# Optimization experiments

Measured on AMD Instinct MI355X. Metric: run time of the kernel, lower is better.

## Reference

```python
import jax, jax.numpy as jnp
import numpy as np

N_OER, N_CONCEPT, N_CLASS = 100000, 20000, 1000
F_ENT, HID = 64, 128
E_SR, E_EP, E_COV, E_BEL = 200000, 400000, 400000, 100000
NEG_SLOPE = 0.2


def _edges(k, n_src, n_dst, e):
    k1, k2 = jax.random.split(k)
    return jnp.stack([jax.random.randint(k1, (e,), 0, n_src),
                      jax.random.randint(k2, (e,), 0, n_dst)]).astype(jnp.int32)


def setup_inputs() -> dict:
    key = jax.random.key(0)
    ks = jax.random.split(key, 24)
    s = 0.05  # small init scale for numerically stable attention logits
    inp = {
        'x_oer': jax.random.normal(ks[0], (N_OER, F_ENT), jnp.float32),
        'x_concept': jax.random.normal(ks[1], (N_CONCEPT, F_ENT), jnp.float32),
        'x_class': jax.random.normal(ks[2], (N_CLASS, F_ENT), jnp.float32),
        'e_oer': jax.random.uniform(ks[3], (N_OER, F_ENT), jnp.float32),
        'e_concept': jax.random.uniform(ks[4], (N_CONCEPT, F_ENT), jnp.float32),
        'e_class': jax.random.uniform(ks[5], (N_CLASS, F_ENT), jnp.float32),
        'W_lin': jax.random.normal(ks[6], (3, F_ENT, HID), jnp.float32) * s,
        'b_lin': jnp.zeros((3, HID), jnp.float32),
        'Wsrc': jax.random.normal(ks[7], (2, 5, HID, HID), jnp.float32) * s,
        'Wdst': jax.random.normal(ks[8], (2, 5, HID, HID), jnp.float32) * s,
        'att_src': jax.random.normal(ks[9], (2, 5, HID), jnp.float32) * s,
        'att_dst': jax.random.normal(ks[10], (2, 5, HID), jnp.float32) * s,
        'b_gat': jnp.zeros((2, 5, HID), jnp.float32),
        'W_cls': jax.random.normal(ks[11], (2 * (F_ENT + HID), 1), jnp.float32) * s,
        'b_cls': jnp.zeros((1,), jnp.float32),
        'ei_before_sr': _edges(ks[12], N_OER, N_OER, E_SR),
        'ei_covers': _edges(ks[14], N_OER, N_CONCEPT, E_COV),
        'ei_belongs': _edges(ks[15], N_CONCEPT, N_CLASS, E_BEL),
        'ei_rev_covers': _edges(ks[16], N_CONCEPT, N_OER, E_COV),
        'ei_rev_belongs': _edges(ks[17], N_CLASS, N_CONCEPT, E_BEL),
    }
    # before_ep edges guaranteed self-loop-free (PyG removes then re-adds self loops)
    k1, k2 = jax.random.split(ks[13])
    src = jax.random.randint(k1, (E_EP,), 0, N_OER)
    dst = (src + jax.random.randint(k2, (E_EP,), 1, N_OER)) % N_OER
    inp['ei_before_ep'] = jnp.stack([src, dst]).astype(jnp.int32)
    return inp


def _gat(x_src, x_dst, src, dst, Ws, Wd, a_s, a_d, b, n_dst):
    # PyG GATConv, heads=1: h = xW (no bias); alpha = softmax_dst(leaky_relu(a_s.h_s[i] + a_d.h_d[j]))
    h_s = x_src @ Ws                                   # [Ns, C]
    h_d = x_dst @ Wd                                   # [Nd, C]
    logit = jax.nn.leaky_relu((h_s @ a_s)[src] + (h_d @ a_d)[dst], NEG_SLOPE)  # [E]
    m = jax.ops.segment_max(logit, dst, num_segments=n_dst)
    ex = jnp.exp(logit - m[dst])
    denom = jax.ops.segment_sum(ex, dst, num_segments=n_dst)
    alpha = ex / denom[dst]
    out = jax.ops.segment_sum(h_s[src] * alpha[:, None], dst, num_segments=n_dst)
    return out + b


def _forward(x_oer, x_concept, x_class, e_oer, e_concept, e_class,
             W_lin, b_lin, Wsrc, Wdst, att_src, att_dst, b_gat, W_cls, b_cls,
             ei_before_sr, ei_before_ep, ei_covers, ei_belongs,
             ei_rev_covers, ei_rev_belongs):
    # per-node-type input projection of the random embeddings
    h_oer = e_oer @ W_lin[0] + b_lin[0]
    h_con = e_concept @ W_lin[1] + b_lin[1]
    h_cls = e_class @ W_lin[2] + b_lin[2]

    # add self loops for OER->OER 'before_ep' (add_self_loops=True)
    loop = jnp.arange(N_OER, dtype=jnp.int32)
    ep_src = jnp.concatenate([ei_before_ep[0], loop])
    ep_dst = jnp.concatenate([ei_before_ep[1], loop])

    for l in range(2):
        P = lambda r: (Wsrc[l, r], Wdst[l, r], att_src[l, r], att_dst[l, r], b_gat[l, r])
        o_ep = _gat(h_oer, h_oer, ep_src, ep_dst, *P(0), N_OER)
        o_cov = _gat(h_oer, h_con, ei_covers[0], ei_covers[1], *P(1), N_CONCEPT)
        o_bel = _gat(h_con, h_cls, ei_belongs[0], ei_belongs[1], *P(2), N_CLASS)
        o_rcov = _gat(h_con, h_oer, ei_rev_covers[0], ei_rev_covers[1], *P(3), N_OER)
        o_rbel = _gat(h_cls, h_con, ei_rev_belongs[0], ei_rev_belongs[1], *P(4), N_CONCEPT)
        # HeteroConv aggr='mean' over edge types per destination node type
        h_oer = (o_ep + o_rcov) * 0.5
        h_con = (o_cov + o_rbel) * 0.5
        h_cls = o_bel

    n_oer = jnp.concatenate([x_oer, h_oer], axis=1)          # [N_OER, F_ENT+HID]
    feat = jnp.concatenate([n_oer[ei_before_sr[0]], n_oer[ei_before_sr[1]]], axis=1)
    return (feat @ W_cls + b_cls)[:, 0]                      # [E_SR]


def reference(x_oer, x_concept, x_class, e_oer, e_concept, e_class,
              W_lin, b_lin, Wsrc, Wdst, att_src, att_dst, b_gat, W_cls, b_cls,
              ei_before_sr, ei_before_ep, ei_covers, ei_belongs,
              ei_rev_covers, ei_rev_belongs):
    return _forward(x_oer, x_concept, x_class, e_oer, e_concept, e_class,
                    W_lin, b_lin, Wsrc, Wdst, att_src, att_dst, b_gat, W_cls, b_cls,
                    ei_before_sr, ei_before_ep, ei_covers, ei_belongs,
                    ei_rev_covers, ei_rev_belongs)
```

## Files before the change

kernel.cpp:

```cpp
#include <hip/hip_runtime.h>
#include <hip/hip_bf16.h>

#define NOER 100000
#define NCON 20000
#define NCLS 1000
#define FENT 64
#define HID 128
#define ESR 200000
#define EEP 400000
#define ECOV 400000
#define EBEL 100000
#define NEG 0.2f
#define NB_TOT 121000

#define SL0 0
#define SL1 NOER
#define SL2 (2*NOER)
#define SL3 (2*NOER + NCON)
#define SL4 (2*NOER + 2*NCON)
#define SL_TOT (2*NOER + 2*NCON + NCLS)
#define DL0 0
#define DL1 NOER
#define DL2 (NOER + NCON)
#define DL3 (NOER + NCON + NCLS)
#define DL4 (2*NOER + NCON + NCLS)
#define DL_TOT (2*NOER + 2*NCON + NCLS)
#define EX_TOT 1500000
#define SCAN_B1 ((DL_TOT + 255) / 256)

#define BSH 9
#define BWID (1 << BSH)
#define NBUCK ((DL_TOT + BWID - 1) / BWID)
#define EPB 4096
#define ABLK ((EX_TOT + EPB - 1) / EPB)

typedef unsigned short u16;
typedef unsigned int u32;
typedef short v8s __attribute__((ext_vector_type(8)));
typedef float v4f __attribute__((ext_vector_type(4)));

__device__ __forceinline__ float b2f(u32 bits) { return __uint_as_float(bits << 16); }
__device__ __forceinline__ u16 f2b(float x) {
    __hip_bfloat16 h = __float2bfloat16(x);
    return *(u16*)&h;
}
__device__ __forceinline__ float wredsum(float p) {
#pragma unroll
    for (int off = 32; off; off >>= 1) p += __shfl_down(p, off);
    return p;
}

__device__ __forceinline__ void edge_decode(int e, const int* __restrict__ ep,
                                            const int* __restrict__ cov,
                                            const int* __restrict__ bel,
                                            const int* __restrict__ rcov,
                                            const int* __restrict__ rbel,
                                            int& s, int& g) {
    if (e < 500000) {
        if (e < EEP) { s = ep[e]; g = DL0 + ep[EEP + e]; }
        else { s = e - EEP; g = DL0 + s; }
    } else if (e < 900000)  { int i = e - 500000;  s = cov[i];  g = DL1 + cov[ECOV + i]; }
    else if (e < 1000000)   { int i = e - 900000;  s = bel[i];  g = DL2 + bel[EBEL + i]; }
    else if (e < 1400000)   { int i = e - 1000000; s = rcov[i]; g = DL3 + rcov[ECOV + i]; }
    else                    { int i = e - 1400000; s = rbel[i]; g = DL4 + rbel[EBEL + i]; }
}

__global__ __launch_bounds__(256) void k_cntA(const int* __restrict__ ep, const int* __restrict__ cov,
                                              const int* __restrict__ bel, const int* __restrict__ rcov,
                                              const int* __restrict__ rbel, int* __restrict__ counts,
                                              int* __restrict__ bhm) {
    __shared__ int lh[NBUCK];
    for (int i = threadIdx.x; i < NBUCK; i += 256) lh[i] = 0;
    __syncthreads();
    int e0 = blockIdx.x * EPB;
    for (int k = 0; k < EPB; k += 256) {
        int e = e0 + k + threadIdx.x;
        if (e < EX_TOT) {
            int s, g;
            edge_decode(e, ep, cov, bel, rcov, rbel, s, g);
            atomicAdd(counts + g, 1);
            atomicAdd(&lh[g >> BSH], 1);
        }
    }
    __syncthreads();
    for (int i = threadIdx.x; i < NBUCK; i += 256) bhm[i * ABLK + blockIdx.x] = lh[i];
}

__global__ void k_scan1(const int* __restrict__ counts, int* __restrict__ part,
                        int* __restrict__ bsum) {
    __shared__ int sm[256];
    int i = blockIdx.x * 256 + threadIdx.x;
    int v = (i < DL_TOT) ? counts[i] : 0;
    sm[threadIdx.x] = v;
    __syncthreads();
#pragma unroll
    for (int off = 1; off < 256; off <<= 1) {
        int x = (threadIdx.x >= off) ? sm[threadIdx.x - off] : 0;
        __syncthreads();
        sm[threadIdx.x] += x;
        __syncthreads();
    }
    if (i < DL_TOT) part[i] = sm[threadIdx.x];
    if (threadIdx.x == 255) bsum[blockIdx.x] = sm[255];
}

__global__ void k_scan2(int* __restrict__ bsum) {
    __shared__ int sm[1024];
    int t = threadIdx.x;
    sm[t] = (t < SCAN_B1) ? bsum[t] : 0;
    __syncthreads();
#pragma unroll
    for (int off = 1; off < 1024; off <<= 1) {
        int x = (t >= off) ? sm[t - off] : 0;
        __syncthreads();
        sm[t] += x;
        __syncthreads();
    }
    if (t < SCAN_B1) bsum[t] = sm[t];
}

__global__ void k_scan3(const int* __restrict__ part, const int* __restrict__ bsum,
                        const int* __restrict__ counts, int* __restrict__ S,
                        int* __restrict__ cursor) {
    int i = blockIdx.x * 256 + threadIdx.x;
    if (i >= DL_TOT) return;
    int b = blockIdx.x;
    int s = part[i] + (b > 0 ? bsum[b - 1] : 0);
    S[i] = s;
    cursor[i] = s - counts[i];
}

__global__ void k_bscanA(const int* __restrict__ bhm, const int* __restrict__ cursor,
                         int* __restrict__ starts) {
    __shared__ int sm[256];
    __shared__ int carry;
    int u = blockIdx.x, t = threadIdx.x;
    if (t == 0) carry = 0;
    __syncthreads();
    int base = cursor[u << BSH];
    for (int c0 = 0; c0 < ABLK; c0 += 256) {
        int i = c0 + t;
        int v = (i < ABLK) ? bhm[u * ABLK + i] : 0;
        sm[t] = v;
        __syncthreads();
#pragma unroll
        for (int off = 1; off < 256; off <<= 1) {
            int x = (t >= off) ? sm[t - off] : 0;
            __syncthreads();
            sm[t] += x;
            __syncthreads();
        }
        if (i < ABLK) starts[u * ABLK + i] = base + carry + sm[t] - v;
        __syncthreads();
        if (t == 255) carry += sm[255];
        __syncthreads();
    }
}

__global__ __launch_bounds__(256) void k_bfillA(const int* __restrict__ ep, const int* __restrict__ cov,
                                                const int* __restrict__ bel, const int* __restrict__ rcov,
                                                const int* __restrict__ rbel,
                                                const int* __restrict__ starts, uint2* __restrict__ pairs) {
    __shared__ int lh[NBUCK];
    for (int i = threadIdx.x; i < NBUCK; i += 256) lh[i] = starts[i * ABLK + blockIdx.x];
    __syncthreads();
    int e0 = blockIdx.x * EPB;
    for (int k = 0; k < EPB; k += 256) {
        int e = e0 + k + threadIdx.x;
        if (e < EX_TOT) {
            int s, g;
            edge_decode(e, ep, cov, bel, rcov, rbel, s, g);
            int pos = atomicAdd(&lh[g >> BSH], 1);
            pairs[pos] = make_uint2((u32)s, (u32)g);
        }
    }
}

__global__ void k_fill2(const uint2* __restrict__ pairs, int* __restrict__ cursor,
                        int* __restrict__ csr) {
    int i = blockIdx.x * blockDim.x + threadIdx.x;
    if (i >= EX_TOT) return;
    uint2 p = pairs[i];
    int pos = atomicAdd(cursor + p.y, 1);
    csr[pos] = (int)p.x;
}

__device__ __forceinline__ int deg_bin(int d) { int b = d > 63 ? 63 : d; return 63 - b; }

__global__ void k_hist2(const int* __restrict__ counts, int* __restrict__ bh) {
    __shared__ int lh[64];
    if (threadIdx.x < 64) lh[threadIdx.x] = 0;
    __syncthreads();
    int g = blockIdx.x * 256 + threadIdx.x;
    if (g < DL_TOT) atomicAdd(&lh[deg_bin(counts[g])], 1);
    __syncthreads();
    if (threadIdx.x < 64) bh[threadIdx.x * SCAN_B1 + blockIdx.x] = lh[threadIdx.x];
}

__global__ void k_bscan(const int* __restrict__ bh, int* __restrict__ boff,
                        int* __restrict__ bintot) {
    __shared__ int sm[256];
    __shared__ int carry;
    int bin = blockIdx.x;
    if (threadIdx.x == 0) carry = 0;
    __syncthreads();
    for (int c0 = 0; c0 < SCAN_B1; c0 += 256) {
        int i = c0 + threadIdx.x;
        int v = (i < SCAN_B1) ? bh[bin * SCAN_B1 + i] : 0;
        sm[threadIdx.x] = v;
        __syncthreads();
#pragma unroll
        for (int off = 1; off < 256; off <<= 1) {
            int x = (threadIdx.x >= off) ? sm[threadIdx.x - off] : 0;
            __syncthreads();
            sm[threadIdx.x] += x;
            __syncthreads();
        }
        if (i < SCAN_B1) boff[bin * SCAN_B1 + i] = carry + sm[threadIdx.x] - v;
        __syncthreads();
        if (threadIdx.x == 255) carry += sm[255];
        __syncthreads();
    }
    if (threadIdx.x == 0) bintot[bin] = carry;
}

__global__ void k_hscan(const int* __restrict__ hist, int* __restrict__ bcur) {
    int t = threadIdx.x;
    int h = hist[t];
    int v = h;
#pragma unroll
    for (int off = 1; off < 64; off <<= 1) {
        int x = __shfl_up(v, off);
        if (t >= off) v += x;
    }
    bcur[t] = v - h;
}

__global__ void k_perm2(const int* __restrict__ counts, const int* __restrict__ binbase,
                        const int* __restrict__ boff, const int* __restrict__ S,
                        int* __restrict__ perm, int* __restrict__ segbeg,
                        int* __restrict__ segend) {
    __shared__ int lh[64];
    if (threadIdx.x < 64)
        lh[threadIdx.x] = binbase[threadIdx.x] + boff[threadIdx.x * SCAN_B1 + blockIdx.x];
    __syncthreads();
    int g = blockIdx.x * 256 + threadIdx.x;
    if (g >= DL_TOT) return;
    int c = counts[g];
    int se = S[g];
    int pos = atomicAdd(&lh[deg_bin(c)], 1);
    perm[pos] = g;
    segbeg[pos] = se - c;
    segend[pos] = se;
}

__global__ void k_cast(const float* __restrict__ e_oer, const float* __restrict__ e_con,
                       const float* __restrict__ e_cls, u16* __restrict__ eb) {
    int idx = blockIdx.x * blockDim.x + threadIdx.x;
    int i4 = idx * 4;
    if (i4 >= NB_TOT * FENT) return;
    const float* src;
    if (i4 < 6400000) src = e_oer + i4;
    else if (i4 < 7680000) src = e_con + (i4 - 6400000);
    else src = e_cls + (i4 - 7680000);
    float4 v = *(const float4*)src;
    u16* d = eb + i4;
    d[0] = f2b(v.x); d[1] = f2b(v.y); d[2] = f2b(v.z); d[3] = f2b(v.w);
}

__global__ void k_prep(const float* __restrict__ W_lin, const float* __restrict__ Wsrc,
                       const float* __restrict__ b_gat,
                       u16* __restrict__ Wlt, u16* __restrict__ Woer, u16* __restrict__ Wcon,
                       u16* __restrict__ Wcls, float* __restrict__ boer,
                       float* __restrict__ bcon, float* __restrict__ bcls2) {
    int i = blockIdx.x * 256 + threadIdx.x;
    if (i < 24576) {
        int t = i / 8192, r = i % 8192, c = r >> 6, k = r & 63;
        Wlt[i] = f2b(W_lin[t * 8192 + k * 128 + c]);
        return;
    }
    i -= 24576;
    if (i < 65536) {
        int l = i >> 15, r = i & 32767, c = r >> 8, k2 = r & 255;
        int rel = 5 * l + (k2 < 128 ? 0 : 3), k = k2 & 127;
        Woer[i] = f2b(Wsrc[(size_t)rel * 16384 + k * 128 + c]);
        return;
    }
    i -= 65536;
    if (i < 65536) {
        int l = i >> 15, r = i & 32767, c = r >> 8, k2 = r & 255;
        int rel = 5 * l + (k2 < 128 ? 1 : 4), k = k2 & 127;
        Wcon[i] = f2b(Wsrc[(size_t)rel * 16384 + k * 128 + c]);
        return;
    }
    i -= 65536;
    if (i < 32768) {
        int l = i >> 14, r = i & 16383, c = r >> 7, k = r & 127;
        Wcls[i] = f2b(Wsrc[(size_t)(5 * l + 2) * 16384 + k * 128 + c]);
        return;
    }
    i -= 32768;
    if (i < 256) { int l = i >> 7, c = i & 127;
        boer[i] = 0.5f * (b_gat[(5 * l + 0) * 128 + c] + b_gat[(5 * l + 3) * 128 + c]); return; }
    i -= 256;
    if (i < 256) { int l = i >> 7, c = i & 127;
        bcon[i] = 0.5f * (b_gat[(5 * l + 1) * 128 + c] + b_gat[(5 * l + 4) * 128 + c]); return; }
    i -= 256;
    if (i < 256) { int l = i >> 7, c = i & 127;
        bcls2[i] = b_gat[(5 * l + 2) * 128 + c]; }
}

__global__ void k_wvec(const float* __restrict__ Wsrc, const float* __restrict__ as_,
                       const float* __restrict__ Wdst, const float* __restrict__ ad,
                       float* __restrict__ wsv, float* __restrict__ wdv) {
    int a = blockIdx.x >> 5;
    int r = ((blockIdx.x & 31) << 2) + (threadIdx.x >> 6);
    int lane = threadIdx.x & 63;
    const float *W, *v;
    float* o;
    if (a < 10) { W = Wsrc + (size_t)a * HID * HID; v = as_ + a * HID; o = wsv + a * HID; }
    else { W = Wdst + (size_t)(a - 10) * HID * HID; v = ad + (a - 10) * HID; o = wdv + (a - 10) * HID; }
    float p = W[r * HID + lane] * v[lane] + W[r * HID + 64 + lane] * v[64 + lane];
    p = wredsum(p);
    if (lane == 0) o[r] = p;
}

struct GemmJob {
    const u16* A0;
    const u16* A1;
    const u16* Wt;
    const float* bias;
    float scale;
    int n, K;
    u16* out;
};

__global__ __launch_bounds__(256) void k_mgemm(GemmJob j0, GemmJob j1, GemmJob j2,
                                               int nb0, int nb1) {
    __shared__ u16 lA[64][40];
    __shared__ u16 lB[128][40];
    GemmJob J;
    int b = blockIdx.x;
    if (b < nb0) J = j0;
    else if (b < nb0 + nb1) { J = j1; b -= nb0; }
    else { J = j2; b -= nb0 + nb1; }
    const int row0 = b * 64;
    const int tid = threadIdx.x, lane = tid & 63, w = tid >> 6;
    const int wr = w >> 1, wc = w & 1;
    const int fr = lane & 15, kg = lane >> 4;
    const int astride = J.A1 ? 128 : J.K;
    v4f acc[2][4];
#pragma unroll
    for (int i = 0; i < 2; ++i)
#pragma unroll
        for (int c = 0; c < 4; ++c) acc[i][c] = (v4f){0.f, 0.f, 0.f, 0.f};

    for (int k0 = 0; k0 < J.K; k0 += 32) {
        const u16* Asrc; int kk;
        if (k0 < 128) { Asrc = J.A0; kk = k0; } else { Asrc = J.A1; kk = k0 - 128; }
        __syncthreads();
        {
            int r = tid >> 2, seg = tid & 3;
            int gr = row0 + r;
            uint4 u = make_uint4(0u, 0u, 0u, 0u);
            if (gr < J.n) u = *(const uint4*)(Asrc + (size_t)gr * astride + kk + seg * 8);
            *(uint4*)&lA[r][seg * 8] = u;
        }
#pragma unroll
        for (int i = 0; i < 2; ++i) {
            int m = tid * 2 + i, c = m >> 2, seg = m & 3;
            uint4 u = *(const uint4*)(J.Wt + (size_t)c * J.K + k0 + seg * 8);
            *(uint4*)&lB[c][seg * 8] = u;
        }
        __syncthreads();
        v8s a0 = *(const v8s*)&lA[32 * wr + fr][8 * kg];
        v8s a1 = *(const v8s*)&lA[32 * wr + 16 + fr][8 * kg];
#pragma unroll
        for (int c = 0; c < 4; ++c) {
            v8s bf = *(const v8s*)&lB[64 * wc + 16 * c + fr][8 * kg];
            acc[0][c] = __builtin_amdgcn_mfma_f32_16x16x32_bf16(a0, bf, acc[0][c], 0, 0, 0);
            acc[1][c] = __builtin_amdgcn_mfma_f32_16x16x32_bf16(a1, bf, acc[1][c], 0, 0, 0);
        }
    }
#pragma unroll
    for (int i = 0; i < 2; ++i)
#pragma unroll
        for (int c = 0; c < 4; ++c) {
            int col = 64 * wc + 16 * c + fr;
            float bv = J.bias[col];
#pragma unroll
            for (int jj = 0; jj < 4; ++jj) {
                int gr = row0 + 32 * wr + 16 * i + 4 * kg + jj;
                if (gr < J.n) J.out[(size_t)gr * 128 + col] = f2b(acc[i][c][jj] * J.scale + bv);
            }
        }
}

__global__ void k_dots_all(const u16* __restrict__ hb, const float* __restrict__ wsv,
                           const float* __restrict__ wdv, float* __restrict__ slp,
                           float* __restrict__ dlp, int lb) {
    int t = blockIdx.x * blockDim.x + threadIdx.x;
    int n = t >> 6, lane = t & 63;
    if (n >= NB_TOT) return;
    const u32* h;
    int m;
    const float *v0, *v1, *v2, *v3;
    float *o0, *o1, *o2, *o3;
    if (n < NOER) {
        m = n; h = (const u32*)hb;
        v0 = wsv + (lb + 0) * HID; o0 = slp + SL0 + m;
        v1 = wsv + (lb + 1) * HID; o1 = slp + SL1 + m;
        v2 = wdv + (lb + 0) * HID; o2 = dlp + DL0 + m;
        v3 = wdv + (lb + 3) * HID; o3 = dlp + DL3 + m;
    } else if (n < NOER + NCON) {
        m = n - NOER; h = (const u32*)(hb + (size_t)NOER * HID);
        v0 = wsv + (lb + 2) * HID; o0 = slp + SL2 + m;
        v1 = wsv + (lb + 3) * HID; o1 = slp + SL3 + m;
        v2 = wdv + (lb + 1) * HID; o2 = dlp + DL1 + m;
        v3 = wdv + (lb + 4) * HID; o3 = dlp + DL4 + m;
    } else {
        m = n - NOER - NCON; h = (const u32*)(hb + (size_t)(NOER + NCON) * HID);
        v0 = wsv + (lb + 4) * HID; o0 = slp + SL4 + m;
        v1 = wdv + (lb + 2) * HID; o1 = dlp + DL2 + m;
        v2 = nullptr; o2 = nullptr; v3 = nullptr; o3 = nullptr;
    }
    u32 hu = h[(size_t)m * 64 + lane];
    float h0 = b2f(hu & 0xffffu), h1 = b2f(hu >> 16);
    float p0 = 0.f, p1 = 0.f, p2 = 0.f, p3 = 0.f;
    { float2 a = *(const float2*)(v0 + 2 * lane); p0 = h0 * a.x + h1 * a.y; }
    { float2 a = *(const float2*)(v1 + 2 * lane); p1 = h0 * a.x + h1 * a.y; }
    if (v2) { float2 a = *(const float2*)(v2 + 2 * lane); p2 = h0 * a.x + h1 * a.y; }
    if (v3) { float2 a = *(const float2*)(v3 + 2 * lane); p3 = h0 * a.x + h1 * a.y; }
    p0 = wredsum(p0); p1 = wredsum(p1); p2 = wredsum(p2); p3 = wredsum(p3);
    if (lane == 0) {
        o0[0] = p0; o1[0] = p1;
        if (o2) o2[0] = p2;
        if (o3) o3[0] = p3;
    }
}

__global__ __launch_bounds__(256) void k_agg_all(const int* __restrict__ csr,
                                                 const int* __restrict__ perm,
                                                 const int* __restrict__ segbeg,
                                                 const int* __restrict__ segend,
                                                 const float* __restrict__ slp,
                                                 const float* __restrict__ dlp,
                                                 const u16* __restrict__ hb,
                                                 u16* __restrict__ tmp) {
    int gi = blockIdx.x * 16 + (threadIdx.x >> 4);
    if (gi >= DL_TOT) return;
    int g = perm[gi];
    int beg = segbeg[gi];
    int end = segend[gi];
    int lane = threadIdx.x & 63;
    int ks = lane & 15;
    int grpbase = lane & 48;
    int c4 = ks * 4;
    const u32* h;
    int sb;
    if (g < DL1)      { h = (const u32*)hb; sb = SL0; }
    else if (g < DL2) { h = (const u32*)hb; sb = SL1; }
    else if (g < DL3) { h = (const u32*)(hb + (size_t)NOER * HID); sb = SL2; }
    else if (g < DL4) { h = (const u32*)(hb + (size_t)NOER * HID); sb = SL3; }
    else              { h = (const u32*)(hb + (size_t)(NOER + NCON) * HID); sb = SL4; }
    float dlv = dlp[g];
    const u32* hc = h + c4;
    float acc[8] = {};
    float denp = 0.f;
    for (int c0 = beg; c0 < end; c0 += 16) {
        int nch = end - c0;
        if (nch > 16) nch = 16;
        int s_l = 0;
        float ex_l = 0.f;
        if (ks < nch) {
            s_l = csr[c0 + ks];
            float lg = slp[sb + s_l] + dlv;
            lg = lg > 0.f ? lg : NEG * lg;
            ex_l = __expf(lg);
            denp += ex_l;
        }
        uint4 hu[16];
#pragma unroll
        for (int j = 0; j < 16; ++j) {
            if (j < nch) {
                int s = __shfl(s_l, grpbase + j);
                hu[j] = *(const uint4*)(hc + ((size_t)s << 6));
            }
        }
#pragma unroll
        for (int j = 0; j < 16; ++j) {
            if (j < nch) {
                float ex = __shfl(ex_l, grpbase + j);
#pragma unroll
                for (int q = 0; q < 4; ++q) {
                    u32 w = ((const u32*)&hu[j])[q];
                    acc[2 * q]     = fmaf(ex, __uint_as_float(w << 16), acc[2 * q]);
                    acc[2 * q + 1] = fmaf(ex, __uint_as_float(w & 0xffff0000u), acc[2 * q + 1]);
                }
            }
        }
    }
    denp += __shfl_xor(denp, 8);
    denp += __shfl_xor(denp, 4);
    denp += __shfl_xor(denp, 2);
    denp += __shfl_xor(denp, 1);
    float inv = (end > beg) ? 1.f / denp : 0.f;
    uint4 r;
    r.x = (u32)f2b(acc[0] * inv) | ((u32)f2b(acc[1] * inv) << 16);
    r.y = (u32)f2b(acc[2] * inv) | ((u32)f2b(acc[3] * inv) << 16);
    r.z = (u32)f2b(acc[4] * inv) | ((u32)f2b(acc[5] * inv) << 16);
    r.w = (u32)f2b(acc[6] * inv) | ((u32)f2b(acc[7] * inv) << 16);
    *(uint4*)((u32*)tmp + (size_t)g * 64 + c4) = r;
}

__global__ void k_score(const float* __restrict__ x, const u16* __restrict__ hb,
                        const float* __restrict__ Wc, float* __restrict__ s1,
                        float* __restrict__ s2) {
    int t = blockIdx.x * blockDim.x + threadIdx.x;
    int n = t >> 6, lane = t & 63;
    if (n >= NOER) return;
    float xv = x[(size_t)n * FENT + lane];
    u32 hu = ((const u32*)hb)[(size_t)n * 64 + lane];
    float h0 = b2f(hu & 0xffffu), h1 = b2f(hu >> 16);
    float2 wa = *(const float2*)(Wc + 64 + 2 * lane);
    float2 wb = *(const float2*)(Wc + 256 + 2 * lane);
    float p1 = xv * Wc[lane] + h0 * wa.x + h1 * wa.y;
    float p2 = xv * Wc[192 + lane] + h0 * wb.x + h1 * wb.y;
#pragma unroll
    for (int off = 32; off; off >>= 1) { p1 += __shfl_down(p1, off); p2 += __shfl_down(p2, off); }
    if (lane == 0) { s1[n] = p1; s2[n] = p2; }
}

__global__ void k_final(const int* __restrict__ src, const int* __restrict__ dst,
                        const float* __restrict__ s1, const float* __restrict__ s2,
                        const float* __restrict__ bcls, float* __restrict__ out) {
    int e = blockIdx.x * blockDim.x + threadIdx.x;
    if (e >= ESR) return;
    out[e] = s1[src[e]] + s2[dst[e]] + bcls[0];
}

extern "C" void kernel_launch(void* const* d_in, const int* in_sizes, int n_in,
                              void* d_out, int out_size, void* d_ws, size_t ws_size,
                              hipStream_t stream) {
    const float* x_oer   = (const float*)d_in[0];
    const float* e_oer   = (const float*)d_in[3];
    const float* e_con   = (const float*)d_in[4];
    const float* e_cls   = (const float*)d_in[5];
    const float* W_lin   = (const float*)d_in[6];
    const float* b_lin   = (const float*)d_in[7];
    const float* Wsrc    = (const float*)d_in[8];
    const float* Wdst    = (const float*)d_in[9];
    const float* att_src = (const float*)d_in[10];
    const float* att_dst = (const float*)d_in[11];
    const float* b_gat   = (const float*)d_in[12];
    const float* W_cls   = (const float*)d_in[13];
    const float* b_cls   = (const float*)d_in[14];
    const int* ei_sr   = (const int*)d_in[15];
    const int* ei_cov  = (const int*)d_in[16];
    const int* ei_bel  = (const int*)d_in[17];
    const int* ei_rcov = (const int*)d_in[18];
    const int* ei_rbel = (const int*)d_in[19];
    const int* ei_ep   = (const int*)d_in[20];

    float* ws = (float*)d_ws;
    size_t o = 0;
    u16* hb  = (u16*)(ws + o); o += (size_t)NB_TOT * HID / 2;
    u16* eb  = (u16*)(ws + o); o += (size_t)NB_TOT * FENT / 2;
    u16* tmp = (u16*)(ws + o); o += (size_t)DL_TOT * HID / 2;
    float* slp  = ws + o; o += SL_TOT;
    float* dlp  = ws + o; o += DL_TOT;
    float* wsv  = ws + o; o += 10 * HID;
    float* wdv  = ws + o; o += 10 * HID;
    u16* Wlt  = (u16*)(ws + o); o += 3 * HID * FENT / 2;
    u16* Woer = (u16*)(ws + o); o += 2 * HID * 256 / 2;
    u16* Wcon = (u16*)(ws + o); o += 2 * HID * 256 / 2;
    u16* Wcls = (u16*)(ws + o); o += 2 * HID * HID / 2;
    float* boerb = ws + o; o += 2 * HID;
    float* bconb = ws + o; o += 2 * HID;
    float* bcls2 = ws + o; o += 2 * HID;
    float* s1 = ws + o; o += NOER;
    float* s2 = ws + o; o += NOER;
    int* counts = (int*)(ws + o); o += DL_TOT;
    int* part   = (int*)(ws + o); o += DL_TOT;
    int* S      = (int*)(ws + o); o += DL_TOT;
    int* cursor = (int*)(ws + o); o += DL_TOT;
    int* perm   = (int*)(ws + o); o += DL_TOT;
    int* segbeg = (int*)(ws + o); o += DL_TOT;
    int* segend = (int*)(ws + o); o += DL_TOT;
    int* bsum   = (int*)(ws + o); o += 1024;
    int* bhm    = (int*)(ws + o); o += NBUCK * ABLK;
    int* starts = (int*)(ws + o); o += NBUCK * ABLK;
    int* bh     = (int*)(ws + o); o += 64 * SCAN_B1;
    int* boff   = (int*)(ws + o); o += 64 * SCAN_B1;
    int* bintot = (int*)(ws + o); o += 64;
    int* binbase= (int*)(ws + o); o += 64;
    uint2* pairs = (uint2*)(ws + o); o += (size_t)EX_TOT * 2;
    int* csr    = (int*)(ws + o); o += EX_TOT;

    u16* hb_con = hb + (size_t)NOER * HID;
    u16* hb_cls = hb + (size_t)(NOER + NCON) * HID;

    hipMemsetAsync(counts, 0, DL_TOT * sizeof(int), stream);
    k_cntA<<<ABLK, 256, 0, stream>>>(ei_ep, ei_cov, ei_bel, ei_rcov, ei_rbel, counts, bhm);
    k_scan1<<<SCAN_B1, 256, 0, stream>>>(counts, part, bsum);
    k_scan2<<<1, 1024, 0, stream>>>(bsum);
    k_scan3<<<SCAN_B1, 256, 0, stream>>>(part, bsum, counts, S, cursor);
    k_bscanA<<<NBUCK, 256, 0, stream>>>(bhm, cursor, starts);
    k_bfillA<<<ABLK, 256, 0, stream>>>(ei_ep, ei_cov, ei_bel, ei_rcov, ei_rbel, starts, pairs);
    k_fill2<<<(EX_TOT + 255) / 256, 256, 0, stream>>>(pairs, cursor, csr);
    k_hist2<<<SCAN_B1, 256, 0, stream>>>(counts, bh);
    k_bscan<<<64, 256, 0, stream>>>(bh, boff, bintot);
    k_hscan<<<1, 64, 0, stream>>>(bintot, binbase);
    k_perm2<<<SCAN_B1, 256, 0, stream>>>(counts, binbase, boff, S, perm, segbeg, segend);

    k_prep<<<739, 256, 0, stream>>>(W_lin, Wsrc, b_gat, Wlt, Woer, Wcon, Wcls, boerb, bconb, bcls2);
    k_cast<<<(NB_TOT * FENT / 4 + 255) / 256, 256, 0, stream>>>(e_oer, e_con, e_cls, eb);
    k_wvec<<<640, 256, 0, stream>>>(Wsrc, att_src, Wdst, att_dst, wsv, wdv);

    {
        GemmJob ja = {eb, nullptr, Wlt, b_lin, 1.f, NOER, FENT, hb};
        GemmJob jb = {eb + (size_t)NOER * FENT, nullptr, Wlt + 8192, b_lin + 128, 1.f, NCON, FENT, hb_con};
        GemmJob jc = {eb + (size_t)(NOER + NCON) * FENT, nullptr, Wlt + 16384, b_lin + 256, 1.f, NCLS, FENT, hb_cls};
        k_mgemm<<<1563 + 313 + 16, 256, 0, stream>>>(ja, jb, jc, 1563, 313);
    }

    for (int l = 0; l < 2; ++l) {
        int lb = l * 5;
        k_dots_all<<<NB_TOT * 64 / 256, 256, 0, stream>>>(hb, wsv, wdv, slp, dlp, lb);
        k_agg_all<<<(DL_TOT + 15) / 16, 256, 0, stream>>>(csr, perm, segbeg, segend, slp, dlp, hb, tmp);
        GemmJob ja = {tmp + (size_t)DL0 * HID, tmp + (size_t)DL3 * HID,
                      Woer + l * 32768, boerb + l * HID, 0.5f, NOER, 256, hb};
        GemmJob jb = {tmp + (size_t)DL1 * HID, tmp + (size_t)DL4 * HID,
                      Wcon + l * 32768, bconb + l * HID, 0.5f, NCON, 256, hb_con};
        GemmJob jc = {tmp + (size_t)DL2 * HID, nullptr,
                      Wcls + l * 16384, bcls2 + l * HID, 1.f, NCLS, 128, hb_cls};
        k_mgemm<<<1563 + 313 + 16, 256, 0, stream>>>(ja, jb, jc, 1563, 313);
    }

    k_score<<<(NOER * 64 + 255) / 256, 256, 0, stream>>>(x_oer, hb, W_cls, s1, s2);
    k_final<<<(ESR + 255) / 256, 256, 0, stream>>>(ei_sr, ei_sr + ESR, s1, s2, b_cls, (float*)d_out);
}
```

Baseline: 479.1 us.

## Fuse attention dot products into GEMM epilogue and enlarge GEMM row tile

Attention logit dot products (source and destination vectors) are now computed in the k_mgemm epilogue from the fp32 accumulators, so the separate k_dots_all pass that re-read the bf16 features is gone. The GEMM row tile doubles to 128 rows per block, giving more MFMA work per B-tile load. The degree histogram is merged into k_scan1, removing k_hist2, and the aggregation output uses nontemporal stores. In exchange, the epilogue adds shared-memory atomics and shuffles, and the dots are taken from fp32 values before bf16 rounding, which changes numerics slightly.

```diff
diff --git a/kernel.cpp b/kernel.cpp
--- a/kernel.cpp
+++ b/kernel.cpp
@@ -34,10 +34,15 @@
 #define EPB 4096
 #define ABLK ((EX_TOT + EPB - 1) / EPB)
 
+#define NB_OER ((NOER + 127) / 128)
+#define NB_CON ((NCON + 127) / 128)
+#define NB_CLS ((NCLS + 127) / 128)
+
 typedef unsigned short u16;
 typedef unsigned int u32;
 typedef short v8s __attribute__((ext_vector_type(8)));
 typedef float v4f __attribute__((ext_vector_type(4)));
+typedef u32 v4u __attribute__((ext_vector_type(4)));
 
 __device__ __forceinline__ float b2f(u32 bits) { return __uint_as_float(bits << 16); }
 __device__ __forceinline__ u16 f2b(float x) {
@@ -86,11 +91,17 @@
     for (int i = threadIdx.x; i < NBUCK; i += 256) bhm[i * ABLK + blockIdx.x] = lh[i];
 }
 
+__device__ __forceinline__ int deg_bin(int d) { int b = d > 63 ? 63 : d; return 63 - b; }
+
 __global__ void k_scan1(const int* __restrict__ counts, int* __restrict__ part,
-                        int* __restrict__ bsum) {
+                        int* __restrict__ bsum, int* __restrict__ bh) {
     __shared__ int sm[256];
+    __shared__ int lh[64];
+    if (threadIdx.x < 64) lh[threadIdx.x] = 0;
+    __syncthreads();
     int i = blockIdx.x * 256 + threadIdx.x;
     int v = (i < DL_TOT) ? counts[i] : 0;
+    if (i < DL_TOT) atomicAdd(&lh[deg_bin(v)], 1);
     sm[threadIdx.x] = v;
     __syncthreads();
 #pragma unroll
@@ -102,6 +113,7 @@
     }
     if (i < DL_TOT) part[i] = sm[threadIdx.x];
     if (threadIdx.x == 255) bsum[blockIdx.x] = sm[255];
+    if (threadIdx.x < 64) bh[threadIdx.x * SCAN_B1 + blockIdx.x] = lh[threadIdx.x];
 }
 
 __global__ void k_scan2(int* __restrict__ bsum) {
@@ -183,18 +195,6 @@
     uint2 p = pairs[i];
     int pos = atomicAdd(cursor + p.y, 1);
     csr[pos] = (int)p.x;
-}
-
-__device__ __forceinline__ int deg_bin(int d) { int b = d > 63 ? 63 : d; return 63 - b; }
-
-__global__ void k_hist2(const int* __restrict__ counts, int* __restrict__ bh) {
-    __shared__ int lh[64];
-    if (threadIdx.x < 64) lh[threadIdx.x] = 0;
-    __syncthreads();
-    int g = blockIdx.x * 256 + threadIdx.x;
-    if (g < DL_TOT) atomicAdd(&lh[deg_bin(counts[g])], 1);
-    __syncthreads();
-    if (threadIdx.x < 64) bh[threadIdx.x * SCAN_B1 + blockIdx.x] = lh[threadIdx.x];
 }
 
 __global__ void k_bscan(const int* __restrict__ bh, int* __restrict__ boff,
@@ -333,25 +333,38 @@
     float scale;
     int n, K;
     u16* out;
+    const float* dv0; const float* dv1; const float* dv2; const float* dv3;
+    float* do0; float* do1; float* do2; float* do3;
 };
 
 __global__ __launch_bounds__(256) void k_mgemm(GemmJob j0, GemmJob j1, GemmJob j2,
                                                int nb0, int nb1) {
-    __shared__ u16 lA[64][40];
+    __shared__ u16 lA[128][40];
     __shared__ u16 lB[128][40];
+    __shared__ float dvs[4][HID];
+    __shared__ float pdot[128][4];
     GemmJob J;
     int b = blockIdx.x;
     if (b < nb0) J = j0;
     else if (b < nb0 + nb1) { J = j1; b -= nb0; }
     else { J = j2; b -= nb0 + nb1; }
-    const int row0 = b * 64;
+    const int row0 = b * 128;
     const int tid = threadIdx.x, lane = tid & 63, w = tid >> 6;
     const int wr = w >> 1, wc = w & 1;
     const int fr = lane & 15, kg = lane >> 4;
     const int astride = J.A1 ? 128 : J.K;
-    v4f acc[2][4];
-#pragma unroll
-    for (int i = 0; i < 2; ++i)
+    const bool dots = (J.do0 != nullptr);
+    if (dots) {
+        for (int i = tid; i < 4 * HID; i += 256) {
+            int v = i >> 7, c = i & 127;
+            const float* dv = (v == 0) ? J.dv0 : (v == 1) ? J.dv1 : (v == 2) ? J.dv2 : J.dv3;
+            dvs[v][c] = dv ? dv[c] : 0.f;
+        }
+        for (int i = tid; i < 128 * 4; i += 256) ((float*)pdot)[i] = 0.f;
+    }
+    v4f acc[4][4];
+#pragma unroll
+    for (int i = 0; i < 4; ++i)
 #pragma unroll
         for (int c = 0; c < 4; ++c) acc[i][c] = (v4f){0.f, 0.f, 0.f, 0.f};
 
@@ -359,8 +372,10 @@
         const u16* Asrc; int kk;
         if (k0 < 128) { Asrc = J.A0; kk = k0; } else { Asrc = J.A1; kk = k0 - 128; }
         __syncthreads();
-        {
-            int r = tid >> 2, seg = tid & 3;
+#pragma unroll
+        for (int p = 0; p < 2; ++p) {
+            int m = tid + p * 256;
+            int r = m >> 2, seg = m & 3;
             int gr = row0 + r;
             uint4 u = make_uint4(0u, 0u, 0u, 0u);
             if (gr < J.n) u = *(const uint4*)(Asrc + (size_t)gr * astride + kk + seg * 8);
@@ -373,69 +388,62 @@
             *(uint4*)&lB[c][seg * 8] = u;
         }
         __syncthreads();
-        v8s a0 = *(const v8s*)&lA[32 * wr + fr][8 * kg];
-        v8s a1 = *(const v8s*)&lA[32 * wr + 16 + fr][8 * kg];
+        v8s a[4];
+#pragma unroll
+        for (int i = 0; i < 4; ++i) a[i] = *(const v8s*)&lA[64 * wr + 16 * i + fr][8 * kg];
 #pragma unroll
         for (int c = 0; c < 4; ++c) {
             v8s bf = *(const v8s*)&lB[64 * wc + 16 * c + fr][8 * kg];
-            acc[0][c] = __builtin_amdgcn_mfma_f32_16x16x32_bf16(a0, bf, acc[0][c], 0, 0, 0);
-            acc[1][c] = __builtin_amdgcn_mfma_f32_16x16x32_bf16(a1, bf, acc[1][c], 0, 0, 0);
-        }
-    }
-#pragma unroll
-    for (int i = 0; i < 2; ++i)
+#pragma unroll
+            for (int i = 0; i < 4; ++i)
+                acc[i][c] = __builtin_amdgcn_mfma_f32_16x16x32_bf16(a[i], bf, acc[i][c], 0, 0, 0);
+        }
+    }
+#pragma unroll
+    for (int i = 0; i < 4; ++i)
 #pragma unroll
         for (int c = 0; c < 4; ++c) {
             int col = 64 * wc + 16 * c + fr;
             float bv = J.bias[col];
 #pragma unroll
             for (int jj = 0; jj < 4; ++jj) {
-                int gr = row0 + 32 * wr + 16 * i + 4 * kg + jj;
+                int gr = row0 + 64 * wr + 16 * i + 4 * kg + jj;
                 if (gr < J.n) J.out[(size_t)gr * 128 + col] = f2b(acc[i][c][jj] * J.scale + bv);
             }
         }
-}
-
-__global__ void k_dots_all(const u16* __restrict__ hb, const float* __restrict__ wsv,
-                           const float* __restrict__ wdv, float* __restrict__ slp,
-                           float* __restrict__ dlp, int lb) {
-    int t = blockIdx.x * blockDim.x + threadIdx.x;
-    int n = t >> 6, lane = t & 63;
-    if (n >= NB_TOT) return;
-    const u32* h;
-    int m;
-    const float *v0, *v1, *v2, *v3;
-    float *o0, *o1, *o2, *o3;
-    if (n < NOER) {
-        m = n; h = (const u32*)hb;
-        v0 = wsv + (lb + 0) * HID; o0 = slp + SL0 + m;
-        v1 = wsv + (lb + 1) * HID; o1 = slp + SL1 + m;
-        v2 = wdv + (lb + 0) * HID; o2 = dlp + DL0 + m;
-        v3 = wdv + (lb + 3) * HID; o3 = dlp + DL3 + m;
-    } else if (n < NOER + NCON) {
-        m = n - NOER; h = (const u32*)(hb + (size_t)NOER * HID);
-        v0 = wsv + (lb + 2) * HID; o0 = slp + SL2 + m;
-        v1 = wsv + (lb + 3) * HID; o1 = slp + SL3 + m;
-        v2 = wdv + (lb + 1) * HID; o2 = dlp + DL1 + m;
-        v3 = wdv + (lb + 4) * HID; o3 = dlp + DL4 + m;
-    } else {
-        m = n - NOER - NCON; h = (const u32*)(hb + (size_t)(NOER + NCON) * HID);
-        v0 = wsv + (lb + 4) * HID; o0 = slp + SL4 + m;
-        v1 = wdv + (lb + 2) * HID; o1 = dlp + DL2 + m;
-        v2 = nullptr; o2 = nullptr; v3 = nullptr; o3 = nullptr;
-    }
-    u32 hu = h[(size_t)m * 64 + lane];
-    float h0 = b2f(hu & 0xffffu), h1 = b2f(hu >> 16);
-    float p0 = 0.f, p1 = 0.f, p2 = 0.f, p3 = 0.f;
-    { float2 a = *(const float2*)(v0 + 2 * lane); p0 = h0 * a.x + h1 * a.y; }
-    { float2 a = *(const float2*)(v1 + 2 * lane); p1 = h0 * a.x + h1 * a.y; }
-    if (v2) { float2 a = *(const float2*)(v2 + 2 * lane); p2 = h0 * a.x + h1 * a.y; }
-    if (v3) { float2 a = *(const float2*)(v3 + 2 * lane); p3 = h0 * a.x + h1 * a.y; }
-    p0 = wredsum(p0); p1 = wredsum(p1); p2 = wredsum(p2); p3 = wredsum(p3);
-    if (lane == 0) {
-        o0[0] = p0; o1[0] = p1;
-        if (o2) o2[0] = p2;
-        if (o3) o3[0] = p3;
+    if (dots) {
+#pragma unroll
+        for (int i = 0; i < 4; ++i)
+#pragma unroll
+            for (int jj = 0; jj < 4; ++jj) {
+                int rl = 64 * wr + 16 * i + 4 * kg + jj;
+                float hv[4];
+#pragma unroll
+                for (int c = 0; c < 4; ++c)
+                    hv[c] = acc[i][c][jj] * J.scale + J.bias[64 * wc + 16 * c + fr];
+#pragma unroll
+                for (int v = 0; v < 4; ++v) {
+                    float p = 0.f;
+#pragma unroll
+                    for (int c = 0; c < 4; ++c)
+                        p = fmaf(hv[c], dvs[v][64 * wc + 16 * c + fr], p);
+                    p += __shfl_xor(p, 1);
+                    p += __shfl_xor(p, 2);
+                    p += __shfl_xor(p, 4);
+                    p += __shfl_xor(p, 8);
+                    if (fr == 0) atomicAdd(&pdot[rl][v], p);
+                }
+            }
+        __syncthreads();
+        if (tid < 128) {
+            int gr = row0 + tid;
+            if (gr < J.n) {
+                if (J.do0) J.do0[gr] = pdot[tid][0];
+                if (J.do1) J.do1[gr] = pdot[tid][1];
+                if (J.do2) J.do2[gr] = pdot[tid][2];
+                if (J.do3) J.do3[gr] = pdot[tid][3];
+            }
+        }
     }
 }
 
@@ -505,12 +513,12 @@
     denp += __shfl_xor(denp, 2);
     denp += __shfl_xor(denp, 1);
     float inv = (end > beg) ? 1.f / denp : 0.f;
-    uint4 r;
+    v4u r;
     r.x = (u32)f2b(acc[0] * inv) | ((u32)f2b(acc[1] * inv) << 16);
     r.y = (u32)f2b(acc[2] * inv) | ((u32)f2b(acc[3] * inv) << 16);
     r.z = (u32)f2b(acc[4] * inv) | ((u32)f2b(acc[5] * inv) << 16);
     r.w = (u32)f2b(acc[6] * inv) | ((u32)f2b(acc[7] * inv) << 16);
-    *(uint4*)((u32*)tmp + (size_t)g * 64 + c4) = r;
+    __builtin_nontemporal_store(r, (v4u*)((u32*)tmp + (size_t)g * 64 + c4));
 }
 
 __global__ void k_score(const float* __restrict__ x, const u16* __restrict__ hb,
@@ -602,13 +610,12 @@
 
     hipMemsetAsync(counts, 0, DL_TOT * sizeof(int), stream);
     k_cntA<<<ABLK, 256, 0, stream>>>(ei_ep, ei_cov, ei_bel, ei_rcov, ei_rbel, counts, bhm);
-    k_scan1<<<SCAN_B1, 256, 0, stream>>>(counts, part, bsum);
+    k_scan1<<<SCAN_B1, 256, 0, stream>>>(counts, part, bsum, bh);
     k_scan2<<<1, 1024, 0, stream>>>(bsum);
     k_scan3<<<SCAN_B1, 256, 0, stream>>>(part, bsum, counts, S, cursor);
     k_bscanA<<<NBUCK, 256, 0, stream>>>(bhm, cursor, starts);
     k_bfillA<<<ABLK, 256, 0, stream>>>(ei_ep, ei_cov, ei_bel, ei_rcov, ei_rbel, starts, pairs);
     k_fill2<<<(EX_TOT + 255) / 256, 256, 0, stream>>>(pairs, cursor, csr);
-    k_hist2<<<SCAN_B1, 256, 0, stream>>>(counts, bh);
     k_bscan<<<64, 256, 0, stream>>>(bh, boff, bintot);
     k_hscan<<<1, 64, 0, stream>>>(bintot, binbase);
     k_perm2<<<SCAN_B1, 256, 0, stream>>>(counts, binbase, boff, S, perm, segbeg, segend);
@@ -617,24 +624,43 @@
     k_cast<<<(NB_TOT * FENT / 4 + 255) / 256, 256, 0, stream>>>(e_oer, e_con, e_cls, eb);
     k_wvec<<<640, 256, 0, stream>>>(Wsrc, att_src, Wdst, att_dst, wsv, wdv);
 
+    const int NBT = NB_OER + NB_CON + NB_CLS;
+
     {
-        GemmJob ja = {eb, nullptr, Wlt, b_lin, 1.f, NOER, FENT, hb};
-        GemmJob jb = {eb + (size_t)NOER * FENT, nullptr, Wlt + 8192, b_lin + 128, 1.f, NCON, FENT, hb_con};
-        GemmJob jc = {eb + (size_t)(NOER + NCON) * FENT, nullptr, Wlt + 16384, b_lin + 256, 1.f, NCLS, FENT, hb_cls};
-        k_mgemm<<<1563 + 313 + 16, 256, 0, stream>>>(ja, jb, jc, 1563, 313);
+        GemmJob ja = {eb, nullptr, Wlt, b_lin, 1.f, NOER, FENT, hb,
+                      wsv + 0 * HID, wsv + 1 * HID, wdv + 0 * HID, wdv + 3 * HID,
+                      slp + SL0, slp + SL1, dlp + DL0, dlp + DL3};
+        GemmJob jb = {eb + (size_t)NOER * FENT, nullptr, Wlt + 8192, b_lin + 128, 1.f, NCON, FENT, hb_con,
+                      wsv + 2 * HID, wsv + 3 * HID, wdv + 1 * HID, wdv + 4 * HID,
+                      slp + SL2, slp + SL3, dlp + DL1, dlp + DL4};
+        GemmJob jc = {eb + (size_t)(NOER + NCON) * FENT, nullptr, Wlt + 16384, b_lin + 256, 1.f, NCLS, FENT, hb_cls,
+                      wsv + 4 * HID, wdv + 2 * HID, nullptr, nullptr,
+                      slp + SL4, dlp + DL2, nullptr, nullptr};
+        k_mgemm<<<NBT, 256, 0, stream>>>(ja, jb, jc, NB_OER, NB_CON);
     }
 
     for (int l = 0; l < 2; ++l) {
-        int lb = l * 5;
-        k_dots_all<<<NB_TOT * 64 / 256, 256, 0, stream>>>(hb, wsv, wdv, slp, dlp, lb);
         k_agg_all<<<(DL_TOT + 15) / 16, 256, 0, stream>>>(csr, perm, segbeg, segend, slp, dlp, hb, tmp);
+        int nb = (l + 1) * 5;
+        bool nd = (l == 0);
         GemmJob ja = {tmp + (size_t)DL0 * HID, tmp + (size_t)DL3 * HID,
-                      Woer + l * 32768, boerb + l * HID, 0.5f, NOER, 256, hb};
+                      Woer + l * 32768, boerb + l * HID, 0.5f, NOER, 256, hb,
+                      nd ? wsv + (nb + 0) * HID : nullptr, nd ? wsv + (nb + 1) * HID : nullptr,
+                      nd ? wdv + (nb + 0) * HID : nullptr, nd ? wdv + (nb + 3) * HID : nullptr,
+                      nd ? slp + SL0 : nullptr, nd ? slp + SL1 : nullptr,
+                      nd ? dlp + DL0 : nullptr, nd ? dlp + DL3 : nullptr};
         GemmJob jb = {tmp + (size_t)DL1 * HID, tmp + (size_t)DL4 * HID,
-                      Wcon + l * 32768, bconb + l * HID, 0.5f, NCON, 256, hb_con};
+                      Wcon + l * 32768, bconb + l * HID, 0.5f, NCON, 256, hb_con,
+                      nd ? wsv + (nb + 2) * HID : nullptr, nd ? wsv + (nb + 3) * HID : nullptr,
+                      nd ? wdv + (nb + 1) * HID : nullptr, nd ? wdv + (nb + 4) * HID : nullptr,
+                      nd ? slp + SL2 : nullptr, nd ? slp + SL3 : nullptr,
+                      nd ? dlp + DL1 : nullptr, nd ? dlp + DL4 : nullptr};
         GemmJob jc = {tmp + (size_t)DL2 * HID, nullptr,
-                      Wcls + l * 16384, bcls2 + l * HID, 1.f, NCLS, 128, hb_cls};
-        k_mgemm<<<1563 + 313 + 16, 256, 0, stream>>>(ja, jb, jc, 1563, 313);
+                      Wcls + l * 16384, bcls2 + l * HID, 1.f, NCLS, 128, hb_cls,
+                      nd ? wsv + (nb + 4) * HID : nullptr, nd ? wdv + (nb + 2) * HID : nullptr,
+                      nullptr, nullptr,
+                      nd ? slp + SL4 : nullptr, nd ? dlp + DL2 : nullptr, nullptr, nullptr};
+        k_mgemm<<<NBT, 256, 0, stream>>>(ja, jb, jc, NB_OER, NB_CON);
     }
 
     k_score<<<(NOER * 64 + 255) / 256, 256, 0, stream>>>(x_oer, hb, W_cls, s1, s2);
```

Result: faster. 465.2 us (median of 2 runs) (-2.9%).
